# Optimization experiments

Measured on AMD Instinct MI355X. Metric: run time of the kernel, lower is better.

Reference implementation:

```python
import jax, jax.numpy as jnp
import numpy as np


def _pair_table(L):
    # 0,0 0,1 ... upper-triangular (start,end) enumeration, P = L*(L+1)/2
    starts = np.concatenate([np.arange(i + 1) for i in range(L)])
    ends = np.concatenate([np.full(i + 1, i) for i in range(L)])
    return starts.astype(np.int32), ends.astype(np.int32)


def setup_inputs() -> dict:
    key = jax.random.key(0)
    ks = jax.random.split(key, 10)
    B, L, Q, H, T = 8, 384, 64, 256, 9
    p = lambda k, shape: jax.random.normal(k, shape, jnp.float32) * 0.02
    return dict(
        batch_hiddens=jax.random.normal(ks[0], (B, L, H), jnp.float32),
        batch_masks=jnp.ones((B, L), dtype=bool),
        queries=jax.random.normal(ks[1], (B, Q, H), jnp.float32),
        queries_locs=jax.random.uniform(ks[2], (B, Q, 2), jnp.float32) * L,
        queries_logits=jax.random.normal(ks[3], (B, Q, T + 1), jnp.float32),
        Wc=p(ks[4], (H, T + 1)), bc=jnp.zeros((T + 1,), jnp.float32),
        Wq=p(ks[5], (H, 2 * H)), bq=jnp.zeros((2 * H,), jnp.float32),
        Wv=p(ks[6], (H, 2 * H)), bv=jnp.zeros((2 * H,), jnp.float32),
        Wo=p(ks[7], (H, 2)), bo=jnp.zeros((2,), jnp.float32),
        Wf=p(ks[8], (H, 2)), bf=jnp.zeros((2,), jnp.float32),
    )


def reference(batch_hiddens, batch_masks, queries, queries_locs, queries_logits,
              Wc, bc, Wq, bq, Wv, bv, Wo, bo, Wf, bf):
    B, L, H = batch_hiddens.shape
    Q = queries.shape[1]
    starts, ends = _pair_table(L)  # static: L known at trace time

    # label probabilities: softmax(prior logits + classifier(queries))
    labels_pros = jax.nn.softmax(queries_logits + queries @ Wc + bc, axis=-1)

    # biaffine start/end channels
    qh = (queries @ Wq + bq).reshape(B, Q, 2, H)        # [B,Q,2,H]
    ch = (batch_hiddens @ Wv + bv).reshape(B, L, 2, H)  # [B,L,2,H]
    score = jnp.einsum('bqch,bvch->bcqv', qh, ch) / jnp.sqrt(jnp.float32(H))
    score = jnp.where(batch_masks[:, None, None, :], score, -1e8)

    # span score via start/end table gather: [B,Q,P]
    span = score[:, 0][:, :, starts] + score[:, 1][:, :, ends]
    mask_p = batch_masks[:, ends]  # [B,P] valid if end token valid

    # locator: gaussian distribution over spans centered at refined locations
    offset = queries @ Wo + bo                      # [B,Q,2]
    factors = jax.nn.softplus(queries @ Wf + bf)    # [B,Q,2] positive widths
    locs = queries_locs + offset                    # [B,Q,2]
    pairs_f = jnp.stack([jnp.asarray(starts), jnp.asarray(ends)], axis=-1).astype(jnp.float32)  # [P,2]
    d2 = (pairs_f[None, None] - locs[:, :, None]) ** 2          # [B,Q,P,2]
    weight = jnp.exp(-(d2 * factors[:, :, None]).sum(-1))       # [B,Q,P]
    weight = jnp.where(mask_p[:, None, :], weight, 0.0)

    # weighted softmax over spans
    m = jnp.max(span, axis=-1, keepdims=True)
    e = jnp.exp(span - m) * weight
    locs_pros = e / (jnp.sum(e, axis=-1, keepdims=True) + 1e-12)
    return labels_pros, locs_pros
```

## Files before the change

kernel.cpp:

```cpp
#include <hip/hip_runtime.h>
#include <math.h>

#define B_    8
#define L_    384
#define Q_    64
#define H_    256
#define R_    512
#define P_    73920
#define NF4   18480
#define QF4   4620

#define WS_WVT   0
#define WS_HIDT  131072
#define WS_G     917504
#define WS_DOTC  1179648
#define WS_LOCS  1180672
#define WS_FACT  1181696
#define WS_EXEY  1182720

__device__ __forceinline__ void tile_transpose(const float* __restrict__ in,
                                               float* __restrict__ outp,
                                               int M, int N, int mt, int nt,
                                               float* smem ) {
    float (*t)[65] = (float(*)[65])smem;
    int lane = threadIdx.x & 63, row4 = threadIdx.x >> 6;
    int m0 = mt * 64, n0 = nt * 64;
#pragma unroll
    for (int p = 0; p < 16; p++) {
        int m = m0 + p * 4 + row4;
        t[p * 4 + row4][lane] = in[m * N + n0 + lane];
    }
    __syncthreads();
#pragma unroll
    for (int p = 0; p < 16; p++) {
        int n = n0 + p * 4 + row4;
        outp[n * M + m0 + lane] = t[lane][p * 4 + row4];
    }
}

__global__ __launch_bounds__(256) void k_front(const float* __restrict__ hid,
                                               const float* __restrict__ Wv,
                                               float* __restrict__ ws) {
    __shared__ float smem[64 * 65];
    int blk = blockIdx.x;
    if (blk < 192) {
        int b = blk / 24, t = blk % 24;
        int mt = t % 6, nt = t / 6;
        tile_transpose(hid + b * 98304, ws + WS_HIDT + b * 98304, 384, 256, mt, nt, smem);
    } else {
        int t = blk - 192;
        int mt = t % 4, nt = t / 4;
        tile_transpose(Wv, ws + WS_WVT, 256, 512, mt, nt, smem);
    }
}

__global__ __launch_bounds__(512) void k_qhg(const float* __restrict__ queries,
                                             const float* __restrict__ Wq,
                                             const float* __restrict__ bq_p,
                                             const float* __restrict__ bv,
                                             const float* __restrict__ qlocs,
                                             const float* __restrict__ qlogits,
                                             const float* __restrict__ Wc,
                                             const float* __restrict__ bc,
                                             const float* __restrict__ Wo,
                                             const float* __restrict__ bo,
                                             const float* __restrict__ Wf,
                                             const float* __restrict__ bf,
                                             float* __restrict__ ws,
                                             float* __restrict__ out) {
    __shared__ float q[4][256];
    __shared__ float qh[4][512];
    int tid = threadIdx.x;
    int r0 = blockIdx.x * 4;

    for (int i = tid; i < 1024; i += 512)
        q[i >> 8][i & 255] = queries[r0 * 256 + i];
    __syncthreads();

    {
        int j = tid;
        float acc[4] = {0, 0, 0, 0};
        for (int h = 0; h < 256; h += 2) {
            float wa = Wq[h * 512 + j];
            float wb = Wq[(h + 1) * 512 + j];
#pragma unroll
            for (int r = 0; r < 4; r++)
                acc[r] += q[r][h] * wa + q[r][h + 1] * wb;
        }
        float bj = bq_p[j];
#pragma unroll
        for (int r = 0; r < 4; r++) qh[r][j] = acc[r] + bj;
    }
    __syncthreads();

    {
        int c = tid >> 8, h = tid & 255;
        const float* wvt = ws + WS_WVT + c * 65536 + h;
        float acc[4] = {0, 0, 0, 0};
        for (int hp = 0; hp < 256; hp += 2) {
            float w0 = wvt[hp * 256];
            float w1 = wvt[(hp + 1) * 256];
#pragma unroll
            for (int r = 0; r < 4; r++)
                acc[r] += qh[r][c * 256 + hp] * w0 + qh[r][c * 256 + hp + 1] * w1;
        }
#pragma unroll
        for (int r = 0; r < 4; r++)
            ws[WS_G + (r0 + r) * 512 + tid] = acc[r];
    }

    {
        int w = tid >> 6, lane = tid & 63;
        int r = w >> 1, c = w & 1;
        float v = 0.f;
#pragma unroll
        for (int k = 0; k < 4; k++) {
            int h = lane + 64 * k;
            v += qh[r][c * 256 + h] * bv[c * 256 + h];
        }
#pragma unroll
        for (int off = 32; off; off >>= 1) v += __shfl_xor(v, off);
        if (lane == 0) ws[WS_DOTC + (r0 + r) * 2 + c] = v;
    }

    {
        int w = tid >> 6, lane = tid & 63;
        if (w < 4) {
            int r = r0 + w;
            float q0 = q[w][lane];
            float q1 = q[w][lane + 64];
            float q2 = q[w][lane + 128];
            float q3 = q[w][lane + 192];

            float x[10];
#pragma unroll
            for (int t = 0; t < 10; t++) {
                float v = q0 * Wc[lane * 10 + t] + q1 * Wc[(lane + 64) * 10 + t]
                        + q2 * Wc[(lane + 128) * 10 + t] + q3 * Wc[(lane + 192) * 10 + t];
#pragma unroll
                for (int off = 32; off; off >>= 1) v += __shfl_xor(v, off);
                x[t] = qlogits[r * 10 + t] + bc[t] + v;
            }
            float m = -1e30f;
#pragma unroll
            for (int t = 0; t < 10; t++) m = fmaxf(m, x[t]);
            float s = 0.f;
#pragma unroll
            for (int t = 0; t < 10; t++) { x[t] = expf(x[t] - m); s += x[t]; }
            float inv = 1.0f / s;
            if (lane == 0) {
#pragma unroll
                for (int t = 0; t < 10; t++) out[r * 10 + t] = x[t] * inv;
            }

#pragma unroll
            for (int k = 0; k < 2; k++) {
                float vo = q0 * Wo[lane * 2 + k] + q1 * Wo[(lane + 64) * 2 + k]
                         + q2 * Wo[(lane + 128) * 2 + k] + q3 * Wo[(lane + 192) * 2 + k];
                float vf = q0 * Wf[lane * 2 + k] + q1 * Wf[(lane + 64) * 2 + k]
                         + q2 * Wf[(lane + 128) * 2 + k] + q3 * Wf[(lane + 192) * 2 + k];
#pragma unroll
                for (int off = 32; off; off >>= 1) { vo += __shfl_xor(vo, off); vf += __shfl_xor(vf, off); }
                if (lane == 0) {
                    ws[WS_LOCS + r * 2 + k] = qlocs[r * 2 + k] + vo + bo[k];
                    float xx = vf + bf[k];
                    ws[WS_FACT + r * 2 + k] = (xx > 20.f) ? xx : log1pf(expf(xx));
                }
            }
        }
    }
}

__global__ __launch_bounds__(384) void k_prep(const float* __restrict__ ws_c,
                                              float* __restrict__ ws,
                                              const int* __restrict__ mask) {
    __shared__ float g0[256], g1[256];
    __shared__ float s0[384], s1[384];
    __shared__ float Ex[384], Ey[384];
    __shared__ float scal[4];

    int tid = threadIdx.x;
    int r = blockIdx.x;
    int b = r >> 6;

    if (tid < 256) {
        g0[tid] = ws_c[WS_G + r * 512 + tid];
        g1[tid] = ws_c[WS_G + r * 512 + 256 + tid];
    }
    float dotc0 = ws_c[WS_DOTC + r * 2 + 0];
    float dotc1 = ws_c[WS_DOTC + r * 2 + 1];
    float lx = ws_c[WS_LOCS + r * 2 + 0], ly = ws_c[WS_LOCS + r * 2 + 1];
    float fx = ws_c[WS_FACT + r * 2 + 0], fy = ws_c[WS_FACT + r * 2 + 1];
    __syncthreads();

    const float* hT = ws_c + WS_HIDT + b * 98304;
    float s0r, s1r;
    bool mk;
    {
        int v = tid;
        float a0 = 0.f, a1 = 0.f;
        const float* p = hT + v;
#pragma unroll 8
        for (int h = 0; h < 256; h++) {
            float x = p[h * 384];
            a0 += x * g0[h];
            a1 += x * g1[h];
        }
        mk = mask[b * 384 + v] != 0;
        s0r = mk ? (a0 + dotc0) * 0.0625f : -1e8f;
        s1r = mk ? (a1 + dotc1) * 0.0625f : -1e8f;
        s0[v] = s0r;
        s1[v] = s1r;
    }
    __syncthreads();

    if (tid < 64) {
        int l = tid;
        float p[6];
        p[0] = s0[l * 6 + 0];
#pragma unroll
        for (int k = 1; k < 6; k++) p[k] = fmaxf(p[k - 1], s0[l * 6 + k]);
        float run = p[5];
#pragma unroll
        for (int off = 1; off < 64; off <<= 1) {
            float t = __shfl_up(run, off);
            if (l >= off) run = fmaxf(run, t);
        }
        float excl = __shfl_up(run, 1);
        if (l == 0) excl = -1e30f;
        float m0 = __shfl(run, 63);
        float lm = -1e30f, lm1 = -1e30f;
#pragma unroll
        for (int k = 0; k < 6; k++) {
            float pm = fmaxf(excl, p[k]);
            float sv = s1[l * 6 + k];
            lm = fmaxf(lm, sv + pm);
            lm1 = fmaxf(lm1, sv);
        }
#pragma unroll
        for (int off = 1; off < 64; off <<= 1) {
            lm  = fmaxf(lm,  __shfl_xor(lm,  off));
            lm1 = fmaxf(lm1, __shfl_xor(lm1, off));
        }
        if (l == 0) { scal[0] = m0; scal[1] = lm1; scal[2] = lm; }
    }
    __syncthreads();

    float m0 = scal[0], m1 = scal[1], mM = scal[2];
    float exv, eyv;
    {
        int i = tid;
        float ds = (float)i - lx;
        exv = expf(s0r - m0 - fx * ds * ds);
        float de = (float)i - ly;
        eyv = mk ? expf(s1r - m1 - fy * de * de) : 0.f;
        Ex[i] = exv;
        Ey[i] = eyv;
    }
    __syncthreads();

    if (tid < 64) {
        int l = tid;
        float p[6];
        p[0] = Ex[l * 6 + 0];
#pragma unroll
        for (int k = 1; k < 6; k++) p[k] = p[k - 1] + Ex[l * 6 + k];
        float run = p[5];
#pragma unroll
        for (int off = 1; off < 64; off <<= 1) {
            float t = __shfl_up(run, off);
            if (l >= off) run += t;
        }
        float excl = __shfl_up(run, 1);
        if (l == 0) excl = 0.f;
        float s2l = 0.f;
#pragma unroll
        for (int k = 0; k < 6; k++)
            s2l += Ey[l * 6 + k] * (excl + p[k]);
#pragma unroll
        for (int off = 1; off < 64; off <<= 1) s2l += __shfl_xor(s2l, off);
        if (l == 0) {
            float C = expf(m0 + m1 - mM);
            scal[3] = C / (C * s2l + 1e-12f);
        }
    }
    __syncthreads();

    float scale = scal[3];
    float* exr = ws + WS_EXEY + r * 768;
    exr[tid]       = exv;
    exr[384 + tid] = eyv * scale;
}

__global__ __launch_bounds__(256) void k_write(const float* __restrict__ ws,
                                               float* __restrict__ out) {
    __shared__ float exey[768];
    int tid = threadIdx.x;
    int r = blockIdx.x >> 2, q = blockIdx.x & 3;
    const float* exr = ws + WS_EXEY + r * 768;
    for (int i = tid; i < 768; i += 256) exey[i] = exr[i];
    __syncthreads();
    const float* Ex = exey;
    const float* Ey = exey + 384;

    float* ob = out + 5120 + r * 73920;
    int base = q * QF4;
    int end = base + QF4;
    for (int idx = base + tid; idx < end; idx += 256) {
        int p0 = idx << 2;
        int e = (int)((sqrtf(8.f * (float)p0 + 1.f) - 1.f) * 0.5f);
        int tri = (e * (e + 1)) >> 1;
        while (tri > p0) { e--; tri -= (e + 1); }
        while (p0 - tri > e) { tri += (e + 1); e++; }
        int s = p0 - tri;
        float ey = Ey[e];
        float4 v;
        v.x = Ex[s] * ey; if (++s > e) { s = 0; ey = Ey[++e]; }
        v.y = Ex[s] * ey; if (++s > e) { s = 0; ey = Ey[++e]; }
        v.z = Ex[s] * ey; if (++s > e) { s = 0; ey = Ey[++e]; }
        v.w = Ex[s] * ey;
        reinterpret_cast<float4*>(ob)[idx] = v;
    }
}

extern "C" void kernel_launch(void* const* d_in, const int* in_sizes, int n_in,
                              void* d_out, int out_size, void* d_ws, size_t ws_size,
                              hipStream_t stream) {
    const float* hiddens = (const float*)d_in[0];
    const int* masks     = (const int*)d_in[1];
    const float* queries = (const float*)d_in[2];
    const float* qlocs   = (const float*)d_in[3];
    const float* qlogits = (const float*)d_in[4];
    const float* Wc = (const float*)d_in[5];
    const float* bc = (const float*)d_in[6];
    const float* Wq = (const float*)d_in[7];
    const float* bq = (const float*)d_in[8];
    const float* Wv = (const float*)d_in[9];
    const float* bv = (const float*)d_in[10];
    const float* Wo = (const float*)d_in[11];
    const float* bo = (const float*)d_in[12];
    const float* Wf = (const float*)d_in[13];
    const float* bf = (const float*)d_in[14];
    float* out = (float*)d_out;
    float* ws  = (float*)d_ws;

    hipLaunchKernelGGL(k_front, dim3(224),  dim3(256), 0, stream, hiddens, Wv, ws);
    hipLaunchKernelGGL(k_qhg,   dim3(128),  dim3(512), 0, stream,
                       queries, Wq, bq, bv, qlocs, qlogits, Wc, bc, Wo, bo, Wf, bf, ws, out);
    hipLaunchKernelGGL(k_prep,  dim3(512),  dim3(384), 0, stream, ws, ws, masks);
    hipLaunchKernelGGL(k_write, dim3(2048), dim3(256), 0, stream, ws, out);
}
```

Measured before the change: 241.0 us.

## Precompose Wq·Wv^T, precompute span index table, vectorize span writes

Folds the two query projections into one precomputed weight product W2 = Wq·Wv^T, with matching bias terms, so each query needs only a single 256x512 matvec instead of two. The triangular (end,start) decode is precomputed into a table instead of a sqrt plus loops per element. The span writer keeps four shifted copies of Ex in shared memory so aligned float4 reads can be used. k_prep now reads g directly from global memory instead of staging it in shared memory. The cost is a 256x256x512 weight product on every call and some reordering of floating-point sums, and the setup and query kernels are restructured with a new workspace layout.

```diff
diff --git a/kernel.cpp b/kernel.cpp
--- a/kernel.cpp
+++ b/kernel.cpp
@@ -10,162 +10,200 @@
 #define NF4   18480
 #define QF4   4620
 
-#define WS_WVT   0
-#define WS_HIDT  131072
-#define WS_G     917504
-#define WS_DOTC  1179648
-#define WS_LOCS  1180672
-#define WS_FACT  1181696
-#define WS_EXEY  1182720
-
-__device__ __forceinline__ void tile_transpose(const float* __restrict__ in,
-                                               float* __restrict__ outp,
-                                               int M, int N, int mt, int nt,
-                                               float* smem ) {
-    float (*t)[65] = (float(*)[65])smem;
-    int lane = threadIdx.x & 63, row4 = threadIdx.x >> 6;
-    int m0 = mt * 64, n0 = nt * 64;
-#pragma unroll
-    for (int p = 0; p < 16; p++) {
-        int m = m0 + p * 4 + row4;
-        t[p * 4 + row4][lane] = in[m * N + n0 + lane];
-    }
-    __syncthreads();
-#pragma unroll
-    for (int p = 0; p < 16; p++) {
-        int n = n0 + p * 4 + row4;
-        outp[n * M + m0 + lane] = t[lane][p * 4 + row4];
-    }
-}
-
-__global__ __launch_bounds__(256) void k_front(const float* __restrict__ hid,
+#define WS_EXEY  0
+#define WS_W2    0
+#define WS_D     131072
+#define WS_WB    131584
+#define WS_E2    132096
+#define WS_TAB   393216
+#define WS_HIDT  411904
+#define WS_G     1198336
+#define WS_DOTC  1460480
+#define WS_LOCS  1461504
+#define WS_FACT  1462528
+
+__global__ __launch_bounds__(512) void k_setup(const float* __restrict__ hid,
+                                               const float* __restrict__ Wq,
+                                               const float* __restrict__ bq,
                                                const float* __restrict__ Wv,
+                                               const float* __restrict__ bv,
                                                float* __restrict__ ws) {
     __shared__ float smem[64 * 65];
-    int blk = blockIdx.x;
-    if (blk < 192) {
-        int b = blk / 24, t = blk % 24;
-        int mt = t % 6, nt = t / 6;
-        tile_transpose(hid + b * 98304, ws + WS_HIDT + b * 98304, 384, 256, mt, nt, smem);
+    int blk = blockIdx.x, tid = threadIdx.x;
+
+    if (blk < 64) {
+        int h0 = blk * 4;
+        int c = tid >> 8, hv = tid & 255;
+        int cu = __builtin_amdgcn_readfirstlane(c);
+        const float4* wv4  = reinterpret_cast<const float4*>(Wv + hv * 512 + cu * 256);
+        const float4* wq40 = reinterpret_cast<const float4*>(Wq + (h0 + 0) * 512 + cu * 256);
+        const float4* wq41 = reinterpret_cast<const float4*>(Wq + (h0 + 1) * 512 + cu * 256);
+        const float4* wq42 = reinterpret_cast<const float4*>(Wq + (h0 + 2) * 512 + cu * 256);
+        const float4* wq43 = reinterpret_cast<const float4*>(Wq + (h0 + 3) * 512 + cu * 256);
+        float a0 = 0.f, a1 = 0.f, a2 = 0.f, a3 = 0.f;
+        for (int k = 0; k < 64; k++) {
+            float4 wv = wv4[k];
+            float4 w0 = wq40[k]; a0 += wv.x * w0.x + wv.y * w0.y + wv.z * w0.z + wv.w * w0.w;
+            float4 w1 = wq41[k]; a1 += wv.x * w1.x + wv.y * w1.y + wv.z * w1.z + wv.w * w1.w;
+            float4 w2 = wq42[k]; a2 += wv.x * w2.x + wv.y * w2.y + wv.z * w2.z + wv.w * w2.w;
+            float4 w3 = wq43[k]; a3 += wv.x * w3.x + wv.y * w3.y + wv.z * w3.z + wv.w * w3.w;
+        }
+        ws[WS_W2 + (h0 + 0) * 512 + tid] = a0;
+        ws[WS_W2 + (h0 + 1) * 512 + tid] = a1;
+        ws[WS_W2 + (h0 + 2) * 512 + tid] = a2;
+        ws[WS_W2 + (h0 + 3) * 512 + tid] = a3;
+        if (tid < 128) {
+            int c2 = tid >> 6, lane = tid & 63;
+#pragma unroll
+            for (int hh = 0; hh < 4; hh++) {
+                float v = 0.f;
+#pragma unroll
+                for (int k2 = 0; k2 < 4; k2++) {
+                    int hp = lane + 64 * k2;
+                    v += Wq[(h0 + hh) * 512 + c2 * 256 + hp] * bv[c2 * 256 + hp];
+                }
+#pragma unroll
+                for (int off = 32; off; off >>= 1) v += __shfl_xor(v, off);
+                if (lane == 0) ws[WS_WB + c2 * 256 + h0 + hh] = v;
+            }
+        }
+    } else if (blk < 101) {
+        int idx = (blk - 64) * 512 + tid;
+        if (idx < NF4) {
+            int p0 = idx << 2;
+            int e = (int)((sqrtf(8.f * (float)p0 + 1.f) - 1.f) * 0.5f);
+            int tri = (e * (e + 1)) >> 1;
+            while (tri > p0) { e--; tri -= (e + 1); }
+            while (p0 - tri > e) { tri += (e + 1); e++; }
+            int s = p0 - tri;
+            reinterpret_cast<unsigned*>(ws)[WS_TAB + idx] = ((unsigned)e << 16) | (unsigned)s;
+        }
+    } else if (blk == 101) {
+        int c = tid >> 8, hv = tid & 255;
+        int cu = __builtin_amdgcn_readfirstlane(c);
+        const float4* wv4 = reinterpret_cast<const float4*>(Wv + hv * 512 + cu * 256);
+        const float4* bq4 = reinterpret_cast<const float4*>(bq + cu * 256);
+        float a = 0.f;
+        for (int k = 0; k < 64; k++) {
+            float4 wv = wv4[k]; float4 b4 = bq4[k];
+            a += wv.x * b4.x + wv.y * b4.y + wv.z * b4.z + wv.w * b4.w;
+        }
+        ws[WS_D + tid] = a;
+        if (tid < 128) {
+            int c2 = tid >> 6, lane = tid & 63;
+            float v = 0.f;
+#pragma unroll
+            for (int k2 = 0; k2 < 4; k2++) {
+                int hp = lane + 64 * k2;
+                v += bq[c2 * 256 + hp] * bv[c2 * 256 + hp];
+            }
+#pragma unroll
+            for (int off = 32; off; off >>= 1) v += __shfl_xor(v, off);
+            if (lane == 0) ws[WS_E2 + c2] = v;
+        }
     } else {
-        int t = blk - 192;
-        int mt = t % 4, nt = t / 4;
-        tile_transpose(Wv, ws + WS_WVT, 256, 512, mt, nt, smem);
-    }
-}
-
-__global__ __launch_bounds__(512) void k_qhg(const float* __restrict__ queries,
-                                             const float* __restrict__ Wq,
-                                             const float* __restrict__ bq_p,
-                                             const float* __restrict__ bv,
-                                             const float* __restrict__ qlocs,
-                                             const float* __restrict__ qlogits,
-                                             const float* __restrict__ Wc,
-                                             const float* __restrict__ bc,
-                                             const float* __restrict__ Wo,
-                                             const float* __restrict__ bo,
-                                             const float* __restrict__ Wf,
-                                             const float* __restrict__ bf,
-                                             float* __restrict__ ws,
-                                             float* __restrict__ out) {
-    __shared__ float q[4][256];
-    __shared__ float qh[4][512];
+        int t = blk - 102;
+        int b = t / 24, tt = t % 24;
+        int mt = tt % 6, nt = tt / 6;
+        const float* in = hid + b * 98304;
+        float* outp = ws + WS_HIDT + b * 98304;
+        float (*tsm)[65] = (float(*)[65])smem;
+        int lane = tid & 63, row8 = tid >> 6;
+        int m0 = mt * 64, n0 = nt * 64;
+#pragma unroll
+        for (int p = 0; p < 8; p++) {
+            int mr = p * 8 + row8;
+            tsm[mr][lane] = in[(m0 + mr) * 256 + n0 + lane];
+        }
+        __syncthreads();
+#pragma unroll
+        for (int p = 0; p < 8; p++) {
+            int nr = p * 8 + row8;
+            outp[(n0 + nr) * 384 + m0 + lane] = tsm[lane][nr];
+        }
+    }
+}
+
+__global__ __launch_bounds__(512) void k_g(const float* __restrict__ queries,
+                                           const float* __restrict__ qlocs,
+                                           const float* __restrict__ qlogits,
+                                           const float* __restrict__ Wc,
+                                           const float* __restrict__ bc,
+                                           const float* __restrict__ Wo,
+                                           const float* __restrict__ bo,
+                                           const float* __restrict__ Wf,
+                                           const float* __restrict__ bf,
+                                           float* __restrict__ ws,
+                                           float* __restrict__ out) {
     int tid = threadIdx.x;
-    int r0 = blockIdx.x * 4;
-
-    for (int i = tid; i < 1024; i += 512)
-        q[i >> 8][i & 255] = queries[r0 * 256 + i];
-    __syncthreads();
+    int r0 = blockIdx.x * 2;
 
     {
-        int j = tid;
-        float acc[4] = {0, 0, 0, 0};
-        for (int h = 0; h < 256; h += 2) {
-            float wa = Wq[h * 512 + j];
-            float wb = Wq[(h + 1) * 512 + j];
-#pragma unroll
-            for (int r = 0; r < 4; r++)
-                acc[r] += q[r][h] * wa + q[r][h + 1] * wb;
-        }
-        float bj = bq_p[j];
-#pragma unroll
-        for (int r = 0; r < 4; r++) qh[r][j] = acc[r] + bj;
-    }
-    __syncthreads();
-
-    {
-        int c = tid >> 8, h = tid & 255;
-        const float* wvt = ws + WS_WVT + c * 65536 + h;
-        float acc[4] = {0, 0, 0, 0};
-        for (int hp = 0; hp < 256; hp += 2) {
-            float w0 = wvt[hp * 256];
-            float w1 = wvt[(hp + 1) * 256];
-#pragma unroll
-            for (int r = 0; r < 4; r++)
-                acc[r] += qh[r][c * 256 + hp] * w0 + qh[r][c * 256 + hp + 1] * w1;
-        }
-#pragma unroll
-        for (int r = 0; r < 4; r++)
-            ws[WS_G + (r0 + r) * 512 + tid] = acc[r];
-    }
-
-    {
-        int w = tid >> 6, lane = tid & 63;
-        int r = w >> 1, c = w & 1;
+        const float* qa = queries + r0 * 256;
+        const float* qb = qa + 256;
+        const float* w2 = ws + WS_W2 + tid;
+        float a0 = 0.f, a1 = 0.f;
+#pragma unroll 8
+        for (int h = 0; h < 256; h++) {
+            float w = w2[h * 512];
+            a0 += qa[h] * w;
+            a1 += qb[h] * w;
+        }
+        float dj = ws[WS_D + tid];
+        ws[WS_G + r0 * 512 + tid]       = a0 + dj;
+        ws[WS_G + (r0 + 1) * 512 + tid] = a1 + dj;
+    }
+
+    int w = tid >> 6, lane = tid & 63;
+    if (w < 4) {
+        int r = r0 + (w >> 1), c = w & 1;
         float v = 0.f;
 #pragma unroll
         for (int k = 0; k < 4; k++) {
             int h = lane + 64 * k;
-            v += qh[r][c * 256 + h] * bv[c * 256 + h];
+            v += queries[r * 256 + h] * ws[WS_WB + c * 256 + h];
         }
 #pragma unroll
         for (int off = 32; off; off >>= 1) v += __shfl_xor(v, off);
-        if (lane == 0) ws[WS_DOTC + (r0 + r) * 2 + c] = v;
-    }
-
-    {
-        int w = tid >> 6, lane = tid & 63;
-        if (w < 4) {
-            int r = r0 + w;
-            float q0 = q[w][lane];
-            float q1 = q[w][lane + 64];
-            float q2 = q[w][lane + 128];
-            float q3 = q[w][lane + 192];
-
-            float x[10];
-#pragma unroll
-            for (int t = 0; t < 10; t++) {
-                float v = q0 * Wc[lane * 10 + t] + q1 * Wc[(lane + 64) * 10 + t]
-                        + q2 * Wc[(lane + 128) * 10 + t] + q3 * Wc[(lane + 192) * 10 + t];
-#pragma unroll
-                for (int off = 32; off; off >>= 1) v += __shfl_xor(v, off);
-                x[t] = qlogits[r * 10 + t] + bc[t] + v;
-            }
-            float m = -1e30f;
-#pragma unroll
-            for (int t = 0; t < 10; t++) m = fmaxf(m, x[t]);
-            float s = 0.f;
-#pragma unroll
-            for (int t = 0; t < 10; t++) { x[t] = expf(x[t] - m); s += x[t]; }
-            float inv = 1.0f / s;
+        if (lane == 0) ws[WS_DOTC + r * 2 + c] = v + ws[WS_E2 + c];
+    } else if (w < 6) {
+        int r = r0 + (w - 4);
+        const float* qr = queries + r * 256;
+        float q0 = qr[lane], q1 = qr[lane + 64], q2 = qr[lane + 128], q3 = qr[lane + 192];
+
+        float x[10];
+#pragma unroll
+        for (int t = 0; t < 10; t++) {
+            float v = q0 * Wc[lane * 10 + t] + q1 * Wc[(lane + 64) * 10 + t]
+                    + q2 * Wc[(lane + 128) * 10 + t] + q3 * Wc[(lane + 192) * 10 + t];
+#pragma unroll
+            for (int off = 32; off; off >>= 1) v += __shfl_xor(v, off);
+            x[t] = qlogits[r * 10 + t] + bc[t] + v;
+        }
+        float m = -1e30f;
+#pragma unroll
+        for (int t = 0; t < 10; t++) m = fmaxf(m, x[t]);
+        float s = 0.f;
+#pragma unroll
+        for (int t = 0; t < 10; t++) { x[t] = expf(x[t] - m); s += x[t]; }
+        float inv = 1.0f / s;
+        if (lane == 0) {
+#pragma unroll
+            for (int t = 0; t < 10; t++) out[r * 10 + t] = x[t] * inv;
+        }
+
+#pragma unroll
+        for (int k = 0; k < 2; k++) {
+            float vo = q0 * Wo[lane * 2 + k] + q1 * Wo[(lane + 64) * 2 + k]
+                     + q2 * Wo[(lane + 128) * 2 + k] + q3 * Wo[(lane + 192) * 2 + k];
+            float vf = q0 * Wf[lane * 2 + k] + q1 * Wf[(lane + 64) * 2 + k]
+                     + q2 * Wf[(lane + 128) * 2 + k] + q3 * Wf[(lane + 192) * 2 + k];
+#pragma unroll
+            for (int off = 32; off; off >>= 1) { vo += __shfl_xor(vo, off); vf += __shfl_xor(vf, off); }
             if (lane == 0) {
-#pragma unroll
-                for (int t = 0; t < 10; t++) out[r * 10 + t] = x[t] * inv;
-            }
-
-#pragma unroll
-            for (int k = 0; k < 2; k++) {
-                float vo = q0 * Wo[lane * 2 + k] + q1 * Wo[(lane + 64) * 2 + k]
-                         + q2 * Wo[(lane + 128) * 2 + k] + q3 * Wo[(lane + 192) * 2 + k];
-                float vf = q0 * Wf[lane * 2 + k] + q1 * Wf[(lane + 64) * 2 + k]
-                         + q2 * Wf[(lane + 128) * 2 + k] + q3 * Wf[(lane + 192) * 2 + k];
-#pragma unroll
-                for (int off = 32; off; off >>= 1) { vo += __shfl_xor(vo, off); vf += __shfl_xor(vf, off); }
-                if (lane == 0) {
-                    ws[WS_LOCS + r * 2 + k] = qlocs[r * 2 + k] + vo + bo[k];
-                    float xx = vf + bf[k];
-                    ws[WS_FACT + r * 2 + k] = (xx > 20.f) ? xx : log1pf(expf(xx));
-                }
+                ws[WS_LOCS + r * 2 + k] = qlocs[r * 2 + k] + vo + bo[k];
+                float xx = vf + bf[k];
+                ws[WS_FACT + r * 2 + k] = (xx > 20.f) ? xx : log1pf(expf(xx));
             }
         }
     }
@@ -174,7 +212,6 @@
 __global__ __launch_bounds__(384) void k_prep(const float* __restrict__ ws_c,
                                               float* __restrict__ ws,
                                               const int* __restrict__ mask) {
-    __shared__ float g0[256], g1[256];
     __shared__ float s0[384], s1[384];
     __shared__ float Ex[384], Ey[384];
     __shared__ float scal[4];
@@ -183,15 +220,11 @@
     int r = blockIdx.x;
     int b = r >> 6;
 
-    if (tid < 256) {
-        g0[tid] = ws_c[WS_G + r * 512 + tid];
-        g1[tid] = ws_c[WS_G + r * 512 + 256 + tid];
-    }
+    const float* gp = ws_c + WS_G + r * 512;
     float dotc0 = ws_c[WS_DOTC + r * 2 + 0];
     float dotc1 = ws_c[WS_DOTC + r * 2 + 1];
     float lx = ws_c[WS_LOCS + r * 2 + 0], ly = ws_c[WS_LOCS + r * 2 + 1];
     float fx = ws_c[WS_FACT + r * 2 + 0], fy = ws_c[WS_FACT + r * 2 + 1];
-    __syncthreads();
 
     const float* hT = ws_c + WS_HIDT + b * 98304;
     float s0r, s1r;
@@ -203,8 +236,8 @@
 #pragma unroll 8
         for (int h = 0; h < 256; h++) {
             float x = p[h * 384];
-            a0 += x * g0[h];
-            a1 += x * g1[h];
+            a0 += x * gp[h];
+            a1 += x * gp[256 + h];
         }
         mk = mask[b * 384 + v] != 0;
         s0r = mk ? (a0 + dotc0) * 0.0625f : -1e8f;
@@ -294,31 +327,44 @@
 
 __global__ __launch_bounds__(256) void k_write(const float* __restrict__ ws,
                                                float* __restrict__ out) {
-    __shared__ float exey[768];
+    __shared__ alignas(16) float exsh[4][384];
+    __shared__ float eysh[384];
     int tid = threadIdx.x;
     int r = blockIdx.x >> 2, q = blockIdx.x & 3;
     const float* exr = ws + WS_EXEY + r * 768;
-    for (int i = tid; i < 768; i += 256) exey[i] = exr[i];
-    __syncthreads();
-    const float* Ex = exey;
-    const float* Ey = exey + 384;
-
+    for (int i = tid; i < 768; i += 256) {
+        float v = exr[i];
+        if (i < 384) {
+#pragma unroll
+            for (int c = 0; c < 4; c++)
+                if (i >= c) exsh[c][i - c] = v;
+        } else {
+            eysh[i - 384] = v;
+        }
+    }
+    __syncthreads();
+
+    const unsigned* tab = reinterpret_cast<const unsigned*>(ws) + WS_TAB;
     float* ob = out + 5120 + r * 73920;
     int base = q * QF4;
     int end = base + QF4;
     for (int idx = base + tid; idx < end; idx += 256) {
-        int p0 = idx << 2;
-        int e = (int)((sqrtf(8.f * (float)p0 + 1.f) - 1.f) * 0.5f);
-        int tri = (e * (e + 1)) >> 1;
-        while (tri > p0) { e--; tri -= (e + 1); }
-        while (p0 - tri > e) { tri += (e + 1); e++; }
-        int s = p0 - tri;
-        float ey = Ey[e];
+        unsigned t = tab[idx];
+        int e = (int)(t >> 16), s = (int)(t & 0xffffu);
         float4 v;
-        v.x = Ex[s] * ey; if (++s > e) { s = 0; ey = Ey[++e]; }
-        v.y = Ex[s] * ey; if (++s > e) { s = 0; ey = Ey[++e]; }
-        v.z = Ex[s] * ey; if (++s > e) { s = 0; ey = Ey[++e]; }
-        v.w = Ex[s] * ey;
+        if (s + 3 <= e) {
+            float ey = eysh[e];
+            const float4* p4 = reinterpret_cast<const float4*>(&exsh[s & 3][s & ~3]);
+            float4 ex = *p4;
+            v.x = ex.x * ey; v.y = ex.y * ey; v.z = ex.z * ey; v.w = ex.w * ey;
+        } else {
+            int ss = s, ee = e;
+            float ey = eysh[ee];
+            v.x = exsh[0][ss] * ey; if (++ss > ee) { ss = 0; ey = eysh[++ee]; }
+            v.y = exsh[0][ss] * ey; if (++ss > ee) { ss = 0; ey = eysh[++ee]; }
+            v.z = exsh[0][ss] * ey; if (++ss > ee) { ss = 0; ey = eysh[++ee]; }
+            v.w = exsh[0][ss] * ey;
+        }
         reinterpret_cast<float4*>(ob)[idx] = v;
     }
 }
@@ -344,9 +390,9 @@
     float* out = (float*)d_out;
     float* ws  = (float*)d_ws;
 
-    hipLaunchKernelGGL(k_front, dim3(224),  dim3(256), 0, stream, hiddens, Wv, ws);
-    hipLaunchKernelGGL(k_qhg,   dim3(128),  dim3(512), 0, stream,
-                       queries, Wq, bq, bv, qlocs, qlogits, Wc, bc, Wo, bo, Wf, bf, ws, out);
+    hipLaunchKernelGGL(k_setup, dim3(294),  dim3(512), 0, stream, hiddens, Wq, bq, Wv, bv, ws);
+    hipLaunchKernelGGL(k_g,     dim3(256),  dim3(512), 0, stream,
+                       queries, qlocs, qlogits, Wc, bc, Wo, bo, Wf, bf, ws, out);
     hipLaunchKernelGGL(k_prep,  dim3(512),  dim3(384), 0, stream, ws, ws, masks);
     hipLaunchKernelGGL(k_write, dim3(2048), dim3(256), 0, stream, ws, out);
 }
```

New measurement: 239.6 us. About the same (-0.6%).
